# Optimization experiments

Measured on AMD Instinct MI355X. Metric: run time of the kernel, lower is better.

Reference implementation:

```python
import jax, jax.numpy as jnp
import numpy as np

D_IN = 1024
D_OUT = 1024

def setup_inputs() -> dict:
    key = jax.random.key(0)
    k1, k2 = jax.random.split(key)
    x = jax.random.normal(k1, (4, 2048, D_IN), dtype=jnp.float32)
    # Keras 'uniform' initializer: U(-0.05, 0.05); kernel has 4 slices, only 0..2 used
    kernel = jax.random.uniform(k2, (4, D_IN, D_OUT), dtype=jnp.float32, minval=-0.05, maxval=0.05)
    return {"x": x, "kernel": kernel}

def reference(x, kernel):
    # QKV projections: x [b, s, d] @ kernel[i] [d, e]
    WQ = jnp.einsum('bsd,de->bse', x, kernel[0])
    WK = jnp.einsum('bsd,de->bse', x, kernel[1])
    WV = jnp.einsum('bsd,de->bse', x, kernel[2])
    scale = 1.0 / jnp.sqrt(jnp.asarray(D_OUT, dtype=WQ.dtype))
    QK = jnp.einsum('bqe,bke->bqk', WQ, WK) * scale  # [b, s, s]
    A = jax.nn.softmax(QK, axis=-1)
    return jnp.einsum('bqk,bke->bqe', A, WV)  # [b, s, e]
```

## Files before the change

### kernel.cpp

```cpp
#include <hip/hip_runtime.h>
#include <hip/hip_bf16.h>
#include <cstdio>

typedef __bf16  bf16x8 __attribute__((ext_vector_type(8)));
typedef float   f32x4  __attribute__((ext_vector_type(4)));
typedef unsigned short u16;
typedef u16     u16x8  __attribute__((ext_vector_type(8)));
typedef u16     u16x4  __attribute__((ext_vector_type(4)));


__device__ __forceinline__ void gld_lds16(const void* g, void* l) {
  __builtin_amdgcn_global_load_lds(
      (const __attribute__((address_space(1))) unsigned int*)g,
      (__attribute__((address_space(3))) unsigned int*)l,
      16, 0, 0);
}

__device__ __forceinline__ u16 f2bf(float f) {
  union { float f; unsigned int u; } c{f};
  unsigned int u = c.u;
  u += 0x7fffu + ((u >> 16) & 1u);
  return (u16)(u >> 16);
}

__device__ __forceinline__ float bf2f(u16 h) {
  union { unsigned int u; float f; } c{(unsigned int)h << 16};
  return c.f;
}

enum { EPI_QKV = 0, EPI_QK = 1, EPI_PV = 2 };


__global__ __launch_bounds__(256) void prep_kernel(const float* __restrict__ x,
                                                   u16* __restrict__ xbf,
                                                   const float* __restrict__ w,
                                                   u16* __restrict__ wt,
                                                   float* __restrict__ rs) {
  __shared__ float tile[32][33];
  const int bid = blockIdx.x;
  if (bid < 4096) {
    const int i = (bid * 256 + threadIdx.x) * 8;
    float4 a = *(const float4*)(x + i);
    float4 b = *(const float4*)(x + i + 4);
    u16x8 r;
    r[0] = f2bf(a.x); r[1] = f2bf(a.y); r[2] = f2bf(a.z); r[3] = f2bf(a.w);
    r[4] = f2bf(b.x); r[5] = f2bf(b.y); r[6] = f2bf(b.z); r[7] = f2bf(b.w);
    *(u16x8*)(xbf + i) = r;
  } else if (bid < 7168) {
    const int b2 = bid - 4096;
    const int s = b2 >> 10, r = b2 & 1023;
    const int e0 = (r & 31) * 32, d0 = (r >> 5) * 32;
    const int tx = threadIdx.x & 31, ty = threadIdx.x >> 5;
    const float* in = w + (size_t)s * 1048576;
#pragma unroll
    for (int j = 0; j < 4; ++j)
      tile[ty + j * 8][tx] = in[(size_t)(d0 + ty + j * 8) * 1024 + e0 + tx];
    __syncthreads();
    u16* o = wt + (size_t)s * 1048576;
#pragma unroll
    for (int j = 0; j < 4; ++j)
      o[(size_t)(e0 + ty + j * 8) * 1024 + d0 + tx] = f2bf(tile[tx][ty + j * 8]);
  } else {
    const float4 z = {0.f, 0.f, 0.f, 0.f};
#pragma unroll
    for (int j = 0; j < 8; ++j)
      ((float4*)rs)[threadIdx.x + j * 256] = z;
  }
}


__device__ __forceinline__ void stage_half(const u16* __restrict__ g, int ld, int k0,
                                           u16* ldsb, int w, int l) {
  const int srow = l >> 3;
  const int scol = ((l & 7) ^ (srow & 7)) * 8;
#pragma unroll
  for (int q = 0; q < 2; ++q) {
    const int r = w * 16 + q * 8;
    gld_lds16(g + (long)(r + srow) * ld + k0 + scol, (void*)(ldsb + r * 64));
  }
}

template <int EPI>
__global__ __launch_bounds__(512, 2)
void gemm256_bt(const u16* __restrict__ A, const u16* __restrict__ B,
                void* __restrict__ Cv, int K, int lda, int ldb, int ldc,
                long sA, long sB, long sC,
                float* __restrict__ rowsum, u16* __restrict__ auxK, u16* __restrict__ auxV) {
  __shared__ __align__(16) u16 lds[65536];

  const int t = threadIdx.x;
  const int w = t >> 6, l = t & 63;
  const int wm = w >> 2, wn = w & 3;
  const int lr = l & 15, lq = l >> 4;
  const int rsw = l & 7;
  const int bz = blockIdx.z;
  const int m0 = blockIdx.y * 256, n0 = blockIdx.x * 256;
  const u16* Ar = A + (long)bz * sA + (long)m0 * lda;
  const u16* Br = B + (long)bz * sB + (long)n0 * ldb;

  u16* curA = lds;
  u16* curB = lds + 16384;
  u16* nxtA = lds + 32768;
  u16* nxtB = lds + 49152;

  const int nt = K >> 6;

  f32x4 acc[8][4] = {};

  stage_half(Ar,             lda, 0, curA,        w, l);
  stage_half(Br,             ldb, 0, curB,        w, l);
  stage_half(Br + 128 * ldb, ldb, 0, curB + 8192, w, l);
  stage_half(Ar + 128 * lda, lda, 0, curA + 8192, w, l);
  asm volatile("s_waitcnt vmcnt(4)" ::: "memory");
  if (nt > 1) {
    stage_half(Ar,             lda, 64, nxtA,        w, l);
    stage_half(Br,             ldb, 64, nxtB,        w, l);
    stage_half(Br + 128 * ldb, ldb, 64, nxtB + 8192, w, l);
    asm volatile("s_waitcnt vmcnt(6)" ::: "memory");
  } else {
    asm volatile("s_waitcnt vmcnt(0)" ::: "memory");
  }
  __builtin_amdgcn_s_barrier();

  for (int tt = 0; tt < nt; ++tt) {
    const int kc = tt << 6;
    bf16x8 a0[4][2], a1[4][2], b0[2][2], b1[2][2];

#pragma unroll
    for (int mi = 0; mi < 4; ++mi)
#pragma unroll
      for (int j = 0; j < 2; ++j)
        a0[mi][j] = *(const bf16x8*)(curA + (wm * 128 + mi * 16 + lr) * 64 +
                                     (((j * 4 + lq) ^ rsw) * 8));
#pragma unroll
    for (int ni = 0; ni < 2; ++ni)
#pragma unroll
      for (int j = 0; j < 2; ++j)
        b0[ni][j] = *(const bf16x8*)(curB + (wn * 64 + ni * 16 + lr) * 64 +
                                     (((j * 4 + lq) ^ rsw) * 8));
    if (tt + 1 < nt)
      stage_half(Ar + 128 * lda, lda, kc + 64, nxtA + 8192, w, l);
    __builtin_amdgcn_s_barrier();
    asm volatile("s_waitcnt lgkmcnt(0)" ::: "memory");
    __builtin_amdgcn_sched_barrier(0);
    __builtin_amdgcn_s_setprio(1);
#pragma unroll
    for (int mi = 0; mi < 4; ++mi)
#pragma unroll
      for (int ni = 0; ni < 2; ++ni)
#pragma unroll
        for (int j = 0; j < 2; ++j)
          acc[mi][ni] = __builtin_amdgcn_mfma_f32_16x16x32_bf16(a0[mi][j], b0[ni][j], acc[mi][ni], 0, 0, 0);
    __builtin_amdgcn_s_setprio(0);
    __builtin_amdgcn_s_barrier();

#pragma unroll
    for (int ni = 0; ni < 2; ++ni)
#pragma unroll
      for (int j = 0; j < 2; ++j)
        b1[ni][j] = *(const bf16x8*)(curB + (wn * 64 + (ni + 2) * 16 + lr) * 64 +
                                     (((j * 4 + lq) ^ rsw) * 8));
    __builtin_amdgcn_s_barrier();
    asm volatile("s_waitcnt lgkmcnt(0)" ::: "memory");
    __builtin_amdgcn_sched_barrier(0);
    __builtin_amdgcn_s_setprio(1);
#pragma unroll
    for (int mi = 0; mi < 4; ++mi)
#pragma unroll
      for (int ni = 0; ni < 2; ++ni)
#pragma unroll
        for (int j = 0; j < 2; ++j)
          acc[mi][ni + 2] = __builtin_amdgcn_mfma_f32_16x16x32_bf16(a0[mi][j], b1[ni][j], acc[mi][ni + 2], 0, 0, 0);
    __builtin_amdgcn_s_setprio(0);
    __builtin_amdgcn_s_barrier();

#pragma unroll
    for (int mi = 0; mi < 4; ++mi)
#pragma unroll
      for (int j = 0; j < 2; ++j)
        a1[mi][j] = *(const bf16x8*)(curA + (wm * 128 + (mi + 4) * 16 + lr) * 64 +
                                     (((j * 4 + lq) ^ rsw) * 8));
    if (tt + 2 < nt)
      stage_half(Br, ldb, kc + 128, curB, w, l);
    __builtin_amdgcn_s_barrier();
    asm volatile("s_waitcnt lgkmcnt(0)" ::: "memory");
    __builtin_amdgcn_sched_barrier(0);
    __builtin_amdgcn_s_setprio(1);
#pragma unroll
    for (int mi = 0; mi < 4; ++mi)
#pragma unroll
      for (int ni = 0; ni < 2; ++ni)
#pragma unroll
        for (int j = 0; j < 2; ++j)
          acc[mi + 4][ni + 2] = __builtin_amdgcn_mfma_f32_16x16x32_bf16(a1[mi][j], b1[ni][j], acc[mi + 4][ni + 2], 0, 0, 0);
    __builtin_amdgcn_s_setprio(0);
    __builtin_amdgcn_s_barrier();

    if (tt + 2 < nt) {
      stage_half(Br + 128 * ldb, ldb, kc + 128, curB + 8192, w, l);
      stage_half(Ar,             lda, kc + 128, curA,        w, l);
    }
    __builtin_amdgcn_s_barrier();
    __builtin_amdgcn_sched_barrier(0);
    __builtin_amdgcn_s_setprio(1);
#pragma unroll
    for (int mi = 0; mi < 4; ++mi)
#pragma unroll
      for (int ni = 0; ni < 2; ++ni)
#pragma unroll
        for (int j = 0; j < 2; ++j)
          acc[mi + 4][ni] = __builtin_amdgcn_mfma_f32_16x16x32_bf16(a1[mi][j], b0[ni][j], acc[mi + 4][ni], 0, 0, 0);
    __builtin_amdgcn_s_setprio(0);
    if (tt + 2 < nt)      asm volatile("s_waitcnt vmcnt(6)" ::: "memory");
    else if (tt + 1 < nt) asm volatile("s_waitcnt vmcnt(0)" ::: "memory");
    __builtin_amdgcn_s_barrier();

    { u16* x_ = curA; curA = nxtA; nxtA = x_; }
    { u16* y_ = curB; curB = nxtB; nxtB = y_; }
  }

  if (EPI == EPI_QK) {
#pragma unroll
    for (int mi = 0; mi < 8; ++mi) {
#pragma unroll
      for (int i = 0; i < 4; ++i) {
        const int row = m0 + wm * 128 + mi * 16 + lq * 4 + i;
        float rs = 0.f;
#pragma unroll
        for (int ni = 0; ni < 4; ++ni) {
          const int col = n0 + wn * 64 + ni * 16 + lr;
          const u16 h = f2bf(__expf(acc[mi][ni][i] * 0.03125f));
          ((u16*)Cv)[(long)bz * sC + (long)row * ldc + col] = h;
          rs += bf2f(h);
        }
        rs += __shfl_xor(rs, 1, 64);
        rs += __shfl_xor(rs, 2, 64);
        rs += __shfl_xor(rs, 4, 64);
        rs += __shfl_xor(rs, 8, 64);
        if (lr == 0) atomicAdd(rowsum + bz * 2048 + row, rs);
      }
    }
    return;
  }

  if (EPI == EPI_QKV && n0 >= 2048) {
    u16* tp = lds;
    const int e0 = n0 - 2048;
    const long bb = m0 >> 11;
    const int kbase = m0 & 2047;
    u16* vt_base = auxV + bb * 2097152;
#pragma unroll
    for (int h = 0; h < 2; ++h) {
      __syncthreads();
      if ((wn >> 1) == h) {
        const int cb = (wn & 1) * 64;
#pragma unroll
        for (int mi = 0; mi < 8; ++mi) {
          const int row0 = wm * 128 + mi * 16 + lq * 4;
#pragma unroll
          for (int ni = 0; ni < 4; ++ni) {
            const int col = cb + ni * 16 + lr;
            u16x4 v4;
#pragma unroll
            for (int i = 0; i < 4; ++i) v4[i] = f2bf(acc[mi][ni][i]);
            *(u16x4*)(tp + col * 264 + row0) = v4;
          }
        }
      }
      __syncthreads();
#pragma unroll
      for (int q = 0; q < 8; ++q) {
        const int chunk = q * 512 + t;
        const int c = chunk >> 5, r0 = (chunk & 31) * 8;
        u16x8 v = *(const u16x8*)(tp + c * 264 + r0);
        *(u16x8*)(vt_base + (long)(e0 + h * 128 + c) * 2048 + kbase + r0) = v;
      }
    }
    return;
  }

  u16* qkv_out = (n0 < 1024) ? (u16*)Cv : auxK;
  const int nl0 = n0 & 1023;
#pragma unroll
  for (int mi = 0; mi < 8; ++mi) {
#pragma unroll
    for (int i = 0; i < 4; ++i) {
      const int row = m0 + wm * 128 + mi * 16 + lq * 4 + i;
#pragma unroll
      for (int ni = 0; ni < 4; ++ni)
        qkv_out[(long)row * 1024 + nl0 + wn * 64 + ni * 16 + lr] = f2bf(acc[mi][ni][i]);
    }
  }
}


template <int EPI>
__global__ __launch_bounds__(256)
void gemm_bt(const u16* __restrict__ A, const u16* __restrict__ B,
             void* __restrict__ Cv, int K, int lda, int ldb, int ldc,
             long sA, long sB, long sC,
             float* __restrict__ rowsum, u16* __restrict__ auxK, u16* __restrict__ auxV) {
  constexpr int LDS_U16 = (EPI == EPI_QKV) ? (128 * 136) : (128 * 128);
  __shared__ __align__(16) u16 lds[LDS_U16];
  u16* As = lds;
  u16* Bs = lds + 128 * 64;

  const int t = threadIdx.x;
  const int w = t >> 6, l = t & 63;
  const int bz = blockIdx.z;
  const u16* Ab = A + (long)bz * sA;
  const u16* Bb = B + (long)bz * sB;
  const int m0 = blockIdx.y * 128, n0 = blockIdx.x * 128;
  const int wm = w & 1, wn = w >> 1;
  const int lr = l & 15, lq = l >> 4;
  const int srow = l >> 3;
  const int scol = ((l & 7) ^ ((l >> 3) & 7)) * 8;
  const int rsw = l & 7;

  f32x4 acc[4][4] = {};

  for (int k0 = 0; k0 < K; k0 += 64) {
    __syncthreads();
#pragma unroll
    for (int c = 0; c < 4; ++c) {
      const int rb = (w * 4 + c) * 8;
      gld_lds16(Ab + (long)(m0 + rb + srow) * lda + k0 + scol, (void*)(As + rb * 64));
      gld_lds16(Bb + (long)(n0 + rb + srow) * ldb + k0 + scol, (void*)(Bs + rb * 64));
    }
    __syncthreads();
#pragma unroll
    for (int j = 0; j < 2; ++j) {
      bf16x8 af[4], bfr[4];
#pragma unroll
      for (int i = 0; i < 4; ++i) {
        const int ch = ((j * 4 + lq) ^ rsw) * 8;
        af[i]  = *(const bf16x8*)(As + (wm * 64 + i * 16 + lr) * 64 + ch);
        bfr[i] = *(const bf16x8*)(Bs + (wn * 64 + i * 16 + lr) * 64 + ch);
      }
#pragma unroll
      for (int mi = 0; mi < 4; ++mi)
#pragma unroll
        for (int ni = 0; ni < 4; ++ni)
          acc[mi][ni] = __builtin_amdgcn_mfma_f32_16x16x32_bf16(af[mi], bfr[ni], acc[mi][ni], 0, 0, 0);
    }
  }

  if (EPI == EPI_QKV && n0 >= 2048) {
    u16* tp = lds;
    __syncthreads();
#pragma unroll
    for (int mi = 0; mi < 4; ++mi) {
      const int row0 = wm * 64 + mi * 16 + lq * 4;
#pragma unroll
      for (int ni = 0; ni < 4; ++ni) {
        const int col = wn * 64 + ni * 16 + lr;
        u16x4 v4;
#pragma unroll
        for (int i = 0; i < 4; ++i) v4[i] = f2bf(acc[mi][ni][i]);
        *(u16x4*)(tp + col * 136 + row0) = v4;
      }
    }
    __syncthreads();
    const int e0 = n0 - 2048;
    const long bb = m0 >> 11;
    const int kbase = m0 & 2047;
    u16* vt_base = auxV + bb * 2097152;
#pragma unroll
    for (int q = 0; q < 8; ++q) {
      const int chunk = q * 256 + t;
      const int c = chunk >> 4, r0 = (chunk & 15) * 8;
      u16x8 v = *(const u16x8*)(tp + c * 136 + r0);
      *(u16x8*)(vt_base + (long)(e0 + c) * 2048 + kbase + r0) = v;
    }
    return;
  }

  u16* qkv_out = nullptr;
  int nl0 = 0;
  if (EPI == EPI_QKV) {
    qkv_out = (n0 < 1024) ? (u16*)Cv : auxK;
    nl0 = n0 & 1023;
  }

#pragma unroll
  for (int mi = 0; mi < 4; ++mi) {
#pragma unroll
    for (int i = 0; i < 4; ++i) {
      const int row = m0 + wm * 64 + mi * 16 + lq * 4 + i;
      float inv;
      if (EPI == EPI_PV) inv = 1.0f / rowsum[bz * 2048 + row];
      float rs = 0.f;
#pragma unroll
      for (int ni = 0; ni < 4; ++ni) {
        const float val = acc[mi][ni][i];
        if (EPI == EPI_QKV) {
          const int col_l = nl0 + wn * 64 + ni * 16 + lr;
          qkv_out[(long)row * 1024 + col_l] = f2bf(val);
        } else if (EPI == EPI_QK) {
          const int col = n0 + wn * 64 + ni * 16 + lr;
          const u16 h = f2bf(__expf(val * 0.03125f));
          ((u16*)Cv)[(long)bz * sC + (long)row * ldc + col] = h;
          rs += bf2f(h);
        } else {
          const int col = n0 + wn * 64 + ni * 16 + lr;
          ((float*)Cv)[(long)bz * sC + (long)row * ldc + col] = val * inv;
        }
      }
      if (EPI == EPI_QK) {
        rs += __shfl_xor(rs, 1, 64);
        rs += __shfl_xor(rs, 2, 64);
        rs += __shfl_xor(rs, 4, 64);
        rs += __shfl_xor(rs, 8, 64);
        if (lr == 0) atomicAdd(rowsum + bz * 2048 + row, rs);
      }
    }
  }
}


extern "C" void kernel_launch(void* const* d_in, const int* in_sizes, int n_in,
                              void* d_out, int out_size, void* d_ws, size_t ws_size,
                              hipStream_t stream) {
  (void)in_sizes; (void)n_in; (void)out_size;
  const float* x    = (const float*)d_in[0];
  const float* kern = (const float*)d_in[1];
  float* out = (float*)d_out;
  char* ws = (char*)d_ws;
  const size_t MB = 1024 * 1024;
  u16*   xbf  = (u16*)(ws);
  u16*   WT   = (u16*)(ws + 16 * MB);
  u16*   Qc   = (u16*)(ws + 22 * MB);
  u16*   Kc   = (u16*)(ws + 38 * MB);
  u16*   VT   = (u16*)(ws + 54 * MB);
  u16*   SP   = (u16*)(ws + 70 * MB);
  float* RS   = (float*)(ws + 102 * MB);
  if (ws_size < 102 * MB + 32768)
    fprintf(stderr, "WARNING: ws_size %zu too small\n", ws_size);

  prep_kernel<<<7169, 256, 0, stream>>>(x, xbf, kern, WT, RS);
  gemm256_bt<EPI_QKV><<<dim3(12, 32, 1), 512, 0, stream>>>(
      xbf, WT, Qc, 1024, 1024, 1024, 1024, 0, 0, 0, nullptr, Kc, VT);
  gemm256_bt<EPI_QK><<<dim3(8, 8, 4), 512, 0, stream>>>(
      Qc, Kc, SP, 1024, 1024, 1024, 2048,
      2048L * 1024, 2048L * 1024, 2048L * 2048, RS, nullptr, nullptr);
  gemm_bt<EPI_PV><<<dim3(8, 16, 4), 256, 0, stream>>>(
      SP, VT, out, 2048, 2048, 2048, 1024,
      2048L * 2048, 1024L * 2048, 2048L * 1024, RS, nullptr, nullptr);
}
```

Before: 243.4 us.

## Unroll GEMM K-loop by two with constant LDS buffers and split V projection launch

The main GEMM loop is unrolled by two through a KTILE macro, so the double-buffer offsets become compile-time constants instead of swapped pointers. The sched_barrier fences are dropped, which gives the compiler more freedom to schedule. The QKV projection is split into a Q/K launch and a separate V-transpose launch, so the V epilogue specialization is chosen at compile time rather than per block. This trades one extra kernel launch and an implicit nt-even assumption for simpler addressing and no divergent epilogue branch.

```diff
diff --git a/kernel.cpp b/kernel.cpp
--- a/kernel.cpp
+++ b/kernel.cpp
@@ -28,7 +28,7 @@
   return c.f;
 }
 
-enum { EPI_QKV = 0, EPI_QK = 1, EPI_PV = 2 };
+enum { EPI_QKV = 0, EPI_QK = 1, EPI_PV = 2, EPI_VT = 3 };
 
 
 __global__ __launch_bounds__(256) void prep_kernel(const float* __restrict__ x,
@@ -80,6 +80,104 @@
   }
 }
 
+#define KTILE(CA, CB, NA, NB, TT, KC)                                              \
+  do {                                                                             \
+    bf16x8 a0[4][2], a1[4][2], b0[2][2], b1[2][2];                                 \
+                 \
+    _Pragma("unroll")                                                              \
+    for (int mi = 0; mi < 4; ++mi)                                                 \
+      _Pragma("unroll")                                                            \
+      for (int j = 0; j < 2; ++j)                                                  \
+        a0[mi][j] = *(const bf16x8*)(lds + (CA) +                                  \
+                      (wm * 128 + mi * 16 + lr) * 64 + (((j * 4 + lq) ^ rsw) * 8));\
+    _Pragma("unroll")                                                              \
+    for (int ni = 0; ni < 2; ++ni)                                                 \
+      _Pragma("unroll")                                                            \
+      for (int j = 0; j < 2; ++j)                                                  \
+        b0[ni][j] = *(const bf16x8*)(lds + (CB) +                                  \
+                      (wn * 64 + ni * 16 + lr) * 64 + (((j * 4 + lq) ^ rsw) * 8)); \
+    if ((TT) + 1 < nt)                                                             \
+      stage_half(Ar + 128 * lda, lda, (KC) + 64, lds + (NA) + 8192, w, l);         \
+    __builtin_amdgcn_s_barrier();                                                  \
+    asm volatile("s_waitcnt lgkmcnt(0)" ::: "memory");                             \
+    __builtin_amdgcn_s_setprio(1);                                                 \
+    _Pragma("unroll")                                                              \
+    for (int mi = 0; mi < 4; ++mi)                                                 \
+      _Pragma("unroll")                                                            \
+      for (int ni = 0; ni < 2; ++ni)                                               \
+        _Pragma("unroll")                                                          \
+        for (int j = 0; j < 2; ++j)                                                \
+          acc[mi][ni] = __builtin_amdgcn_mfma_f32_16x16x32_bf16(                   \
+              a0[mi][j], b0[ni][j], acc[mi][ni], 0, 0, 0);                         \
+    __builtin_amdgcn_s_setprio(0);                                                 \
+    __builtin_amdgcn_s_barrier();                                                  \
+           \
+    _Pragma("unroll")                                                              \
+    for (int ni = 0; ni < 2; ++ni)                                                 \
+      _Pragma("unroll")                                                            \
+      for (int j = 0; j < 2; ++j)                                                  \
+        b1[ni][j] = *(const bf16x8*)(lds + (CB) +                                  \
+                      (wn * 64 + (ni + 2) * 16 + lr) * 64 +                        \
+                      (((j * 4 + lq) ^ rsw) * 8));                                 \
+    __builtin_amdgcn_s_barrier();                                                  \
+    asm volatile("s_waitcnt lgkmcnt(0)" ::: "memory");                             \
+    __builtin_amdgcn_s_setprio(1);                                                 \
+    _Pragma("unroll")                                                              \
+    for (int mi = 0; mi < 4; ++mi)                                                 \
+      _Pragma("unroll")                                                            \
+      for (int ni = 0; ni < 2; ++ni)                                               \
+        _Pragma("unroll")                                                          \
+        for (int j = 0; j < 2; ++j)                                                \
+          acc[mi][ni + 2] = __builtin_amdgcn_mfma_f32_16x16x32_bf16(               \
+              a0[mi][j], b1[ni][j], acc[mi][ni + 2], 0, 0, 0);                     \
+    __builtin_amdgcn_s_setprio(0);                                                 \
+    __builtin_amdgcn_s_barrier();                                                  \
+                           \
+    _Pragma("unroll")                                                              \
+    for (int mi = 0; mi < 4; ++mi)                                                 \
+      _Pragma("unroll")                                                            \
+      for (int j = 0; j < 2; ++j)                                                  \
+        a1[mi][j] = *(const bf16x8*)(lds + (CA) +                                  \
+                      (wm * 128 + (mi + 4) * 16 + lr) * 64 +                       \
+                      (((j * 4 + lq) ^ rsw) * 8));                                 \
+    if ((TT) + 2 < nt)                                                             \
+      stage_half(Br, ldb, (KC) + 128, lds + (CB), w, l);                           \
+    __builtin_amdgcn_s_barrier();                                                  \
+    asm volatile("s_waitcnt lgkmcnt(0)" ::: "memory");                             \
+    __builtin_amdgcn_s_setprio(1);                                                 \
+    _Pragma("unroll")                                                              \
+    for (int mi = 0; mi < 4; ++mi)                                                 \
+      _Pragma("unroll")                                                            \
+      for (int ni = 0; ni < 2; ++ni)                                               \
+        _Pragma("unroll")                                                          \
+        for (int j = 0; j < 2; ++j)                                                \
+          acc[mi + 4][ni + 2] = __builtin_amdgcn_mfma_f32_16x16x32_bf16(           \
+              a1[mi][j], b1[ni][j], acc[mi + 4][ni + 2], 0, 0, 0);                 \
+    __builtin_amdgcn_s_setprio(0);                                                 \
+    __builtin_amdgcn_s_barrier();                                                  \
+       \
+    if ((TT) + 2 < nt) {                                                           \
+      stage_half(Br + 128 * ldb, ldb, (KC) + 128, lds + (CB) + 8192, w, l);        \
+      stage_half(Ar,             lda, (KC) + 128, lds + (CA),        w, l);        \
+    }                                                                              \
+    __builtin_amdgcn_s_barrier();                                                  \
+    __builtin_amdgcn_s_setprio(1);                                                 \
+    _Pragma("unroll")                                                              \
+    for (int mi = 0; mi < 4; ++mi)                                                 \
+      _Pragma("unroll")                                                            \
+      for (int ni = 0; ni < 2; ++ni)                                               \
+        _Pragma("unroll")                                                          \
+        for (int j = 0; j < 2; ++j)                                                \
+          acc[mi + 4][ni] = __builtin_amdgcn_mfma_f32_16x16x32_bf16(               \
+              a1[mi][j], b0[ni][j], acc[mi + 4][ni], 0, 0, 0);                     \
+    __builtin_amdgcn_s_setprio(0);                                                 \
+    if ((TT) + 2 < nt)                                                             \
+      asm volatile("s_waitcnt vmcnt(6)" ::: "memory");                             \
+    else if ((TT) + 1 < nt)                                                        \
+      asm volatile("s_waitcnt vmcnt(0)" ::: "memory");                             \
+    __builtin_amdgcn_s_barrier();                                                  \
+  } while (0)
+
 template <int EPI>
 __global__ __launch_bounds__(512, 2)
 void gemm256_bt(const u16* __restrict__ A, const u16* __restrict__ B,
@@ -98,125 +196,28 @@
   const u16* Ar = A + (long)bz * sA + (long)m0 * lda;
   const u16* Br = B + (long)bz * sB + (long)n0 * ldb;
 
-  u16* curA = lds;
-  u16* curB = lds + 16384;
-  u16* nxtA = lds + 32768;
-  u16* nxtB = lds + 49152;
-
   const int nt = K >> 6;
 
   f32x4 acc[8][4] = {};
 
-  stage_half(Ar,             lda, 0, curA,        w, l);
-  stage_half(Br,             ldb, 0, curB,        w, l);
-  stage_half(Br + 128 * ldb, ldb, 0, curB + 8192, w, l);
-  stage_half(Ar + 128 * lda, lda, 0, curA + 8192, w, l);
+  stage_half(Ar,             lda, 0, lds,         w, l);
+  stage_half(Br,             ldb, 0, lds + 16384, w, l);
+  stage_half(Br + 128 * ldb, ldb, 0, lds + 24576, w, l);
+  stage_half(Ar + 128 * lda, lda, 0, lds + 8192,  w, l);
   asm volatile("s_waitcnt vmcnt(4)" ::: "memory");
   if (nt > 1) {
-    stage_half(Ar,             lda, 64, nxtA,        w, l);
-    stage_half(Br,             ldb, 64, nxtB,        w, l);
-    stage_half(Br + 128 * ldb, ldb, 64, nxtB + 8192, w, l);
+    stage_half(Ar,             lda, 64, lds + 32768, w, l);
+    stage_half(Br,             ldb, 64, lds + 49152, w, l);
+    stage_half(Br + 128 * ldb, ldb, 64, lds + 57344, w, l);
     asm volatile("s_waitcnt vmcnt(6)" ::: "memory");
   } else {
     asm volatile("s_waitcnt vmcnt(0)" ::: "memory");
   }
   __builtin_amdgcn_s_barrier();
 
-  for (int tt = 0; tt < nt; ++tt) {
-    const int kc = tt << 6;
-    bf16x8 a0[4][2], a1[4][2], b0[2][2], b1[2][2];
-
-#pragma unroll
-    for (int mi = 0; mi < 4; ++mi)
-#pragma unroll
-      for (int j = 0; j < 2; ++j)
-        a0[mi][j] = *(const bf16x8*)(curA + (wm * 128 + mi * 16 + lr) * 64 +
-                                     (((j * 4 + lq) ^ rsw) * 8));
-#pragma unroll
-    for (int ni = 0; ni < 2; ++ni)
-#pragma unroll
-      for (int j = 0; j < 2; ++j)
-        b0[ni][j] = *(const bf16x8*)(curB + (wn * 64 + ni * 16 + lr) * 64 +
-                                     (((j * 4 + lq) ^ rsw) * 8));
-    if (tt + 1 < nt)
-      stage_half(Ar + 128 * lda, lda, kc + 64, nxtA + 8192, w, l);
-    __builtin_amdgcn_s_barrier();
-    asm volatile("s_waitcnt lgkmcnt(0)" ::: "memory");
-    __builtin_amdgcn_sched_barrier(0);
-    __builtin_amdgcn_s_setprio(1);
-#pragma unroll
-    for (int mi = 0; mi < 4; ++mi)
-#pragma unroll
-      for (int ni = 0; ni < 2; ++ni)
-#pragma unroll
-        for (int j = 0; j < 2; ++j)
-          acc[mi][ni] = __builtin_amdgcn_mfma_f32_16x16x32_bf16(a0[mi][j], b0[ni][j], acc[mi][ni], 0, 0, 0);
-    __builtin_amdgcn_s_setprio(0);
-    __builtin_amdgcn_s_barrier();
-
-#pragma unroll
-    for (int ni = 0; ni < 2; ++ni)
-#pragma unroll
-      for (int j = 0; j < 2; ++j)
-        b1[ni][j] = *(const bf16x8*)(curB + (wn * 64 + (ni + 2) * 16 + lr) * 64 +
-                                     (((j * 4 + lq) ^ rsw) * 8));
-    __builtin_amdgcn_s_barrier();
-    asm volatile("s_waitcnt lgkmcnt(0)" ::: "memory");
-    __builtin_amdgcn_sched_barrier(0);
-    __builtin_amdgcn_s_setprio(1);
-#pragma unroll
-    for (int mi = 0; mi < 4; ++mi)
-#pragma unroll
-      for (int ni = 0; ni < 2; ++ni)
-#pragma unroll
-        for (int j = 0; j < 2; ++j)
-          acc[mi][ni + 2] = __builtin_amdgcn_mfma_f32_16x16x32_bf16(a0[mi][j], b1[ni][j], acc[mi][ni + 2], 0, 0, 0);
-    __builtin_amdgcn_s_setprio(0);
-    __builtin_amdgcn_s_barrier();
-
-#pragma unroll
-    for (int mi = 0; mi < 4; ++mi)
-#pragma unroll
-      for (int j = 0; j < 2; ++j)
-        a1[mi][j] = *(const bf16x8*)(curA + (wm * 128 + (mi + 4) * 16 + lr) * 64 +
-                                     (((j * 4 + lq) ^ rsw) * 8));
-    if (tt + 2 < nt)
-      stage_half(Br, ldb, kc + 128, curB, w, l);
-    __builtin_amdgcn_s_barrier();
-    asm volatile("s_waitcnt lgkmcnt(0)" ::: "memory");
-    __builtin_amdgcn_sched_barrier(0);
-    __builtin_amdgcn_s_setprio(1);
-#pragma unroll
-    for (int mi = 0; mi < 4; ++mi)
-#pragma unroll
-      for (int ni = 0; ni < 2; ++ni)
-#pragma unroll
-        for (int j = 0; j < 2; ++j)
-          acc[mi + 4][ni + 2] = __builtin_amdgcn_mfma_f32_16x16x32_bf16(a1[mi][j], b1[ni][j], acc[mi + 4][ni + 2], 0, 0, 0);
-    __builtin_amdgcn_s_setprio(0);
-    __builtin_amdgcn_s_barrier();
-
-    if (tt + 2 < nt) {
-      stage_half(Br + 128 * ldb, ldb, kc + 128, curB + 8192, w, l);
-      stage_half(Ar,             lda, kc + 128, curA,        w, l);
-    }
-    __builtin_amdgcn_s_barrier();
-    __builtin_amdgcn_sched_barrier(0);
-    __builtin_amdgcn_s_setprio(1);
-#pragma unroll
-    for (int mi = 0; mi < 4; ++mi)
-#pragma unroll
-      for (int ni = 0; ni < 2; ++ni)
-#pragma unroll
-        for (int j = 0; j < 2; ++j)
-          acc[mi + 4][ni] = __builtin_amdgcn_mfma_f32_16x16x32_bf16(a1[mi][j], b0[ni][j], acc[mi + 4][ni], 0, 0, 0);
-    __builtin_amdgcn_s_setprio(0);
-    if (tt + 2 < nt)      asm volatile("s_waitcnt vmcnt(6)" ::: "memory");
-    else if (tt + 1 < nt) asm volatile("s_waitcnt vmcnt(0)" ::: "memory");
-    __builtin_amdgcn_s_barrier();
-
-    { u16* x_ = curA; curA = nxtA; nxtA = x_; }
-    { u16* y_ = curB; curB = nxtB; nxtB = y_; }
+  for (int it = 0; it < nt; it += 2) {
+    KTILE(0,     16384, 32768, 49152, it,     it << 6);
+    KTILE(32768, 49152, 0,     16384, it + 1, (it + 1) << 6);
   }
 
   if (EPI == EPI_QK) {
@@ -243,9 +244,9 @@
     return;
   }
 
-  if (EPI == EPI_QKV && n0 >= 2048) {
+  if (EPI == EPI_VT) {
     u16* tp = lds;
-    const int e0 = n0 - 2048;
+    const int e0 = n0;
     const long bb = m0 >> 11;
     const int kbase = m0 & 2047;
     u16* vt_base = auxV + bb * 2097152;
@@ -438,8 +439,11 @@
     fprintf(stderr, "WARNING: ws_size %zu too small\n", ws_size);
 
   prep_kernel<<<7169, 256, 0, stream>>>(x, xbf, kern, WT, RS);
-  gemm256_bt<EPI_QKV><<<dim3(12, 32, 1), 512, 0, stream>>>(
-      xbf, WT, Qc, 1024, 1024, 1024, 1024, 0, 0, 0, nullptr, Kc, VT);
+  gemm256_bt<EPI_QKV><<<dim3(8, 32, 1), 512, 0, stream>>>(
+      xbf, WT, Qc, 1024, 1024, 1024, 1024, 0, 0, 0, nullptr, Kc, nullptr);
+  gemm256_bt<EPI_VT><<<dim3(4, 32, 1), 512, 0, stream>>>(
+      xbf, WT + 2 * 1048576, nullptr, 1024, 1024, 1024, 1024, 0, 0, 0,
+      nullptr, nullptr, VT);
   gemm256_bt<EPI_QK><<<dim3(8, 8, 4), 512, 0, stream>>>(
       Qc, Kc, SP, 1024, 1024, 1024, 2048,
       2048L * 1024, 2048L * 1024, 2048L * 2048, RS, nullptr, nullptr);
```

Measured after the change: 250.0 us. 1.03x slower.
